# Kernel optimization log

Measured on AMD Instinct MI355X. Metric: run time of the kernel, lower is better.

Reference implementation:

```python
import jax, jax.numpy as jnp
import numpy as np

B, S, D = 8, 2048, 1024
NEG = -1000000000.0  # float32 masking constant from original code


def setup_inputs() -> dict:
    key = jax.random.key(0)
    kq, kk, kv, km = jax.random.split(key, 4)
    q = jax.random.normal(kq, (B, S, D), dtype=jnp.float32)
    k = jax.random.normal(kk, (B, S, D), dtype=jnp.float32)
    v = jax.random.normal(kv, (B, S, D), dtype=jnp.float32)
    mask = (jax.random.uniform(km, (B, 1, S)) < 0.1).astype(jnp.float32)
    return {"q": q, "k": k, "v": v, "mask": mask}


def reference(q, k, v, mask):
    scale = jnp.asarray(D ** -0.5, dtype=q.dtype)
    # [B,S,S] = q @ k^T, scaled
    logits = jnp.einsum("bqd,bkd->bqk", q, k) * scale
    logits = logits + mask * NEG  # mask broadcasts over query axis
    attn = jax.nn.softmax(logits, axis=-1)
    return jnp.einsum("bqk,bkd->bqd", attn, v)
```

## Files before the change

kernel.cpp:

```cpp
#include <hip/hip_runtime.h>
#include <hip/hip_bf16.h>

#define NB 8
#define SS 2048
#define DDIM 1024

typedef __attribute__((ext_vector_type(8))) short bf16x8;
typedef __attribute__((ext_vector_type(4))) float f32x4;

__device__ inline void gload_lds16(const void* g, void* l) {
  __builtin_amdgcn_global_load_lds(
      (const __attribute__((address_space(1))) void*)g,
      (__attribute__((address_space(3))) void*)l, 16, 0, 0);
}

__device__ inline ushort f2bf(float f) {
  union { float f; unsigned int u; } v;
  v.f = f;
  unsigned int u = v.u;
  unsigned int r = (u + 0x7FFFu + ((u >> 16) & 1u)) >> 16;
  return (ushort)r;
}

__device__ inline unsigned int pack2(float a, float b) {
  return (unsigned int)f2bf(a) | ((unsigned int)f2bf(b) << 16);
}

__global__ void init_zero(float* __restrict__ p, int n) {
  int i = blockIdx.x * 256 + threadIdx.x;
  if (i < n) p[i] = 0.f;
}

__global__ void conv_bf16(const float* __restrict__ in, ushort* __restrict__ out,
                          int n8) {
  int i = blockIdx.x * 256 + threadIdx.x;
  if (i >= n8) return;
  const float4* p = (const float4*)in + (size_t)i * 2;
  float4 a = p[0], b = p[1];
  uint4 o;
  o.x = pack2(a.x, a.y);
  o.y = pack2(a.z, a.w);
  o.z = pack2(b.x, b.y);
  o.w = pack2(b.z, b.w);
  ((uint4*)out)[i] = o;
}

__global__ void conv_transpose_v(const float* __restrict__ V,
                                 ushort* __restrict__ VT) {
  __shared__ ushort tile[64][65];
  const int b = blockIdx.z;
  const int k0 = blockIdx.x * 64;
  const int d0 = blockIdx.y * 64;
  const float* Vb = V + (size_t)b * SS * DDIM;
  ushort* VTb = VT + (size_t)b * DDIM * SS;
  const int t = threadIdx.x;
#pragma unroll
  for (int i = 0; i < 16; i++) {
    int flat = i * 256 + t;
    int r = flat >> 6, c = flat & 63;
    tile[r][c] = f2bf(Vb[(size_t)(k0 + r) * DDIM + d0 + c]);
  }
  __syncthreads();
#pragma unroll
  for (int i = 0; i < 16; i++) {
    int flat = i * 256 + t;
    int r = flat >> 6, c = flat & 63;
    VTb[(size_t)(d0 + r) * SS + k0 + c] = tile[c][r];
  }
}

template <bool EXPEPI, typename OutT>
__global__ void gemm_bt(const ushort* __restrict__ A, const ushort* __restrict__ Bm,
                        OutT* __restrict__ C, const float* __restrict__ maskp,
                        float* __restrict__ rowsum, int M, int N, int K,
                        float alpha) {
  __shared__ ushort lA[128 * 32];
  __shared__ ushort lB[128 * 32];
  const int tid = threadIdx.x;
  const int wave = tid >> 6, lane = tid & 63;
  const int quad = lane >> 4, l16 = lane & 15;
  const int wm = wave >> 1, wn = wave & 1;
  const int b = blockIdx.z;
  const ushort* Ab = A + (size_t)b * M * K;
  const ushort* Bb = Bm + (size_t)b * N * K;
  const int tileM = blockIdx.y * 128, tileN = blockIdx.x * 128;

  f32x4 acc[4][4];
#pragma unroll
  for (int i = 0; i < 4; i++)
#pragma unroll
    for (int j = 0; j < 4; j++) acc[i][j] = (f32x4){0.f, 0.f, 0.f, 0.f};

  for (int k0 = 0; k0 < K; k0 += 32) {
#pragma unroll
    for (int c = 0; c < 2; c++) {
      int flat = (wave * 2 + c) * 1024 + lane * 16;
      int row = flat >> 6, kb = flat & 63;
      gload_lds16((const char*)Ab + ((size_t)(tileM + row) * K + k0) * 2 + kb,
                  (char*)lA + flat);
      gload_lds16((const char*)Bb + ((size_t)(tileN + row) * K + k0) * 2 + kb,
                  (char*)lB + flat);
    }
    asm volatile("s_waitcnt vmcnt(0)" ::: "memory");
    __syncthreads();

    bf16x8 af[4], bfr[4];
#pragma unroll
    for (int mi = 0; mi < 4; mi++)
      af[mi] = *(const bf16x8*)((const char*)lA +
                                ((wm * 64 + mi * 16 + l16) * 32 + quad * 8) * 2);
#pragma unroll
    for (int ni = 0; ni < 4; ni++)
      bfr[ni] = *(const bf16x8*)((const char*)lB +
                                 ((wn * 64 + ni * 16 + l16) * 32 + quad * 8) * 2);
#pragma unroll
    for (int mi = 0; mi < 4; mi++)
#pragma unroll
      for (int ni = 0; ni < 4; ni++)
        acc[mi][ni] = __builtin_amdgcn_mfma_f32_16x16x32_bf16(af[mi], bfr[ni],
                                                              acc[mi][ni], 0, 0, 0);
    __syncthreads();
  }

  OutT* Cb = C + (size_t)b * M * N;
  if (EXPEPI) {
    const float* mb = maskp + (size_t)b * N;
    float mv[4];
#pragma unroll
    for (int ni = 0; ni < 4; ni++)
      mv[ni] = mb[tileN + wn * 64 + ni * 16 + l16] * (-1e9f);
#pragma unroll
    for (int mi = 0; mi < 4; mi++) {
#pragma unroll
      for (int r = 0; r < 4; r++) {
        int row = tileM + wm * 64 + mi * 16 + quad * 4 + r;
        float s = 0.f;
#pragma unroll
        for (int ni = 0; ni < 4; ni++) {
          int col = tileN + wn * 64 + ni * 16 + l16;
          float e = __expf(acc[mi][ni][r] * alpha + mv[ni]);
          ((ushort*)Cb)[(size_t)row * N + col] = f2bf(e);
          s += e;
        }
        s += __shfl_xor(s, 1, 64);
        s += __shfl_xor(s, 2, 64);
        s += __shfl_xor(s, 4, 64);
        s += __shfl_xor(s, 8, 64);
        if (l16 == 0) atomicAdd(&rowsum[(size_t)b * M + row], s);
      }
    }
  } else {
#pragma unroll
    for (int mi = 0; mi < 4; mi++) {
      float inv[4];
#pragma unroll
      for (int r = 0; r < 4; r++) {
        int row = tileM + wm * 64 + mi * 16 + quad * 4 + r;
        inv[r] = 1.0f / rowsum[(size_t)b * M + row];
      }
#pragma unroll
      for (int ni = 0; ni < 4; ni++) {
        int col = tileN + wn * 64 + ni * 16 + l16;
#pragma unroll
        for (int r = 0; r < 4; r++) {
          int row = tileM + wm * 64 + mi * 16 + quad * 4 + r;
          ((float*)Cb)[(size_t)row * N + col] = acc[mi][ni][r] * alpha * inv[r];
        }
      }
    }
  }
}

extern "C" void kernel_launch(void* const* d_in, const int* in_sizes, int n_in,
                              void* d_out, int out_size, void* d_ws, size_t ws_size,
                              hipStream_t stream) {
  const float* q = (const float*)d_in[0];
  const float* k = (const float*)d_in[1];
  const float* v = (const float*)d_in[2];
  const float* mask = (const float*)d_in[3];
  float* out = (float*)d_out;

  const size_t pQ = (size_t)SS * DDIM * 2;
  const size_t pP = (size_t)SS * SS * 2;
  const size_t pR = (size_t)SS * 4;

  int gb = 8;
  while (gb > 1 && (size_t)gb * (3 * pQ + pP + pR) > ws_size) gb >>= 1;

  for (int b0 = 0; b0 < NB; b0 += gb) {
    char* w = (char*)d_ws;
    ushort* qb = (ushort*)w;
    ushort* kb = (ushort*)(w + (size_t)gb * pQ);
    ushort* vtb = (ushort*)(w + (size_t)gb * pQ * 2);
    ushort* Sc = (ushort*)(w + (size_t)gb * pQ * 3);
    float* rowsum = (float*)(w + (size_t)gb * (pQ * 3 + pP));

    const float* qg = q + (size_t)b0 * SS * DDIM;
    const float* kg = k + (size_t)b0 * SS * DDIM;
    const float* vg = v + (size_t)b0 * SS * DDIM;
    const float* mg = mask + (size_t)b0 * SS;
    float* og = out + (size_t)b0 * SS * DDIM;

    const int nrs = gb * SS;
    init_zero<<<(nrs + 255) / 256, 256, 0, stream>>>(rowsum, nrs);
    const int n8 = gb * SS * DDIM / 8;
    conv_bf16<<<n8 / 256, 256, 0, stream>>>(qg, qb, n8);
    conv_bf16<<<n8 / 256, 256, 0, stream>>>(kg, kb, n8);
    conv_transpose_v<<<dim3(SS / 64, DDIM / 64, gb), 256, 0, stream>>>(vg, vtb);
    gemm_bt<true, ushort><<<dim3(SS / 128, SS / 128, gb), 256, 0, stream>>>(
        qb, kb, Sc, mg, rowsum, SS, SS, DDIM, 0.03125f);
    gemm_bt<false, float><<<dim3(DDIM / 128, SS / 128, gb), 256, 0, stream>>>(
        Sc, vtb, og, nullptr, rowsum, SS, DDIM, SS, 1.0f);
  }
}
```

Measured before the change: 412.0 us.

## Rewrite bf16 GEMMs with 256x256 tiles, double-buffered swizzled LDS and phased MFMA pipeline

Both GEMM kernels move from 128x128 tiles with 4 waves to 256x256 tiles with 8 waves. Global-to-LDS loads are double-buffered across 64-wide K steps, and each step is split into four barrier-separated quarter phases so loads for the next step overlap MFMA work. LDS rows are XOR-swizzled to avoid bank conflicts, and workgroup IDs are remapped across XCDs for cache locality. The aim is better data reuse and hiding of memory latency. The cost is 128KB of LDS per block, which limits occupancy to one block per CU, and fewer workgroups for the PV GEMM.

```diff
diff --git a/kernel.cpp b/kernel.cpp
--- a/kernel.cpp
+++ b/kernel.cpp
@@ -69,76 +69,158 @@
   }
 }
 
+#define MFMA16(mh, nh)                                                        \
+  _Pragma("unroll") for (int ks = 0; ks < 2; ks++)                            \
+  _Pragma("unroll") for (int mi = 0; mi < 4; mi++)                            \
+  _Pragma("unroll") for (int ni = 0; ni < 2; ni++)                            \
+      acc[mh][mi][nh][ni] = __builtin_amdgcn_mfma_f32_16x16x32_bf16(          \
+          af[mi][ks], bf[ni][ks], acc[mh][mi][nh][ni], 0, 0, 0);
+
+#define PHASE(mh, nh)                                                         \
+  __builtin_amdgcn_s_barrier();                                               \
+  asm volatile("s_waitcnt lgkmcnt(0)" ::: "memory");                          \
+  __builtin_amdgcn_sched_barrier(0);                                          \
+  __builtin_amdgcn_s_setprio(1);                                              \
+  MFMA16(mh, nh);                                                             \
+  __builtin_amdgcn_s_setprio(0);                                              \
+  __builtin_amdgcn_sched_barrier(0);
+
+#define VMW(n) asm volatile("s_waitcnt vmcnt(" #n ")" ::: "memory")
+#define ENDP() __builtin_amdgcn_s_barrier()
+
+#define RD_A(d, h)                                                            \
+  _Pragma("unroll") for (int mi = 0; mi < 4; mi++) {                          \
+    const char* _p = ldsc + (d) * 65536 + (h) * 16384 + aoff[mi];             \
+    af[mi][0] = *(const bf16x8*)(_p + koff0);                                 \
+    af[mi][1] = *(const bf16x8*)(_p + koff1);                                 \
+  }
+
+#define RD_B(d, h)                                                            \
+  _Pragma("unroll") for (int ni = 0; ni < 2; ni++) {                          \
+    const char* _p = ldsc + (d) * 65536 + 32768 + (h) * 16384 + boff[ni];     \
+    bf[ni][0] = *(const bf16x8*)(_p + koff0);                                 \
+    bf[ni][1] = *(const bf16x8*)(_p + koff1);                                 \
+  }
+
+#define STAGE(dbuf, isB, h, kt_)                                              \
+  do {                                                                        \
+    const ushort* _s = (isB) ? Bb : Ab;                                       \
+    const int _t0 = (isB) ? tileN : tileM;                                    \
+    char* _lb = ldsc + (dbuf) * 65536 + (isB) * 32768 + (h) * 16384;          \
+    gload_lds16(_s + (size_t)(_t0 + (h) * 128 + r0) * K + (kt_) * 64 + c8,    \
+                _lb + ol0);                                                   \
+    gload_lds16(_s + (size_t)(_t0 + (h) * 128 + r1) * K + (kt_) * 64 + c8,    \
+                _lb + ol1);                                                   \
+  } while (0)
+
 template <bool EXPEPI, typename OutT>
-__global__ void gemm_bt(const ushort* __restrict__ A, const ushort* __restrict__ Bm,
-                        OutT* __restrict__ C, const float* __restrict__ maskp,
-                        float* __restrict__ rowsum, int M, int N, int K,
-                        float alpha) {
-  __shared__ ushort lA[128 * 32];
-  __shared__ ushort lB[128 * 32];
+__global__ __launch_bounds__(512, 2) void gemm_bt(
+    const ushort* __restrict__ A, const ushort* __restrict__ Bm,
+    OutT* __restrict__ C, const float* __restrict__ maskp,
+    float* __restrict__ rowsum, int M, int N, int K, float alpha) {
+  __shared__ __attribute__((aligned(128))) char ldsc[131072];
   const int tid = threadIdx.x;
   const int wave = tid >> 6, lane = tid & 63;
   const int quad = lane >> 4, l16 = lane & 15;
-  const int wm = wave >> 1, wn = wave & 1;
-  const int b = blockIdx.z;
+  const int wm = wave >> 2, wn = wave & 3;
+
+  const int gx = gridDim.x, gy = gridDim.y;
+  const int lin = blockIdx.x + gx * (blockIdx.y + gy * blockIdx.z);
+  const int nwg = gx * gy * (int)gridDim.z;
+  const int cpx = nwg >> 3;
+  const int swz = (lin & 7) * cpx + (lin >> 3);
+  const int bz = swz / (gx * gy);
+  const int rem = swz - bz * (gx * gy);
+  const int by = rem / gx;
+  const int bx = rem - by * gx;
+
+  const int b = bz;
   const ushort* Ab = A + (size_t)b * M * K;
   const ushort* Bb = Bm + (size_t)b * N * K;
-  const int tileM = blockIdx.y * 128, tileN = blockIdx.x * 128;
-
-  f32x4 acc[4][4];
-#pragma unroll
-  for (int i = 0; i < 4; i++)
-#pragma unroll
-    for (int j = 0; j < 4; j++) acc[i][j] = (f32x4){0.f, 0.f, 0.f, 0.f};
-
-  for (int k0 = 0; k0 < K; k0 += 32) {
-#pragma unroll
-    for (int c = 0; c < 2; c++) {
-      int flat = (wave * 2 + c) * 1024 + lane * 16;
-      int row = flat >> 6, kb = flat & 63;
-      gload_lds16((const char*)Ab + ((size_t)(tileM + row) * K + k0) * 2 + kb,
-                  (char*)lA + flat);
-      gload_lds16((const char*)Bb + ((size_t)(tileN + row) * K + k0) * 2 + kb,
-                  (char*)lB + flat);
-    }
-    asm volatile("s_waitcnt vmcnt(0)" ::: "memory");
-    __syncthreads();
-
-    bf16x8 af[4], bfr[4];
+  const int tileM = by * 256, tileN = bx * 256;
+
+  const int ol0 = wave * 2048 + lane * 16;
+  const int ol1 = ol0 + 1024;
+  const int r0 = ol0 >> 7;
+  const int r1 = r0 + 8;
+  const int c8 = (((lane & 7) ^ (r0 & 7)) * 8);
+
+  const int x7 = lane & 7;
+  const int koff0 = ((quad) ^ x7) * 16;
+  const int koff1 = ((4 + quad) ^ x7) * 16;
+  int aoff[4], boff[2];
+#pragma unroll
+  for (int mi = 0; mi < 4; mi++) aoff[mi] = (wm * 64 + mi * 16 + l16) * 128;
+#pragma unroll
+  for (int ni = 0; ni < 2; ni++) boff[ni] = (wn * 32 + ni * 16 + l16) * 128;
+
+  f32x4 acc[2][4][2][2];
+#pragma unroll
+  for (int mh = 0; mh < 2; mh++)
 #pragma unroll
     for (int mi = 0; mi < 4; mi++)
-      af[mi] = *(const bf16x8*)((const char*)lA +
-                                ((wm * 64 + mi * 16 + l16) * 32 + quad * 8) * 2);
-#pragma unroll
-    for (int ni = 0; ni < 4; ni++)
-      bfr[ni] = *(const bf16x8*)((const char*)lB +
-                                 ((wn * 64 + ni * 16 + l16) * 32 + quad * 8) * 2);
-#pragma unroll
-    for (int mi = 0; mi < 4; mi++)
-#pragma unroll
-      for (int ni = 0; ni < 4; ni++)
-        acc[mi][ni] = __builtin_amdgcn_mfma_f32_16x16x32_bf16(af[mi], bfr[ni],
-                                                              acc[mi][ni], 0, 0, 0);
-    __syncthreads();
+#pragma unroll
+      for (int nh = 0; nh < 2; nh++)
+#pragma unroll
+        for (int ni = 0; ni < 2; ni++)
+          acc[mh][mi][nh][ni] = (f32x4){0.f, 0.f, 0.f, 0.f};
+
+  bf16x8 af[4][2], bf[2][2];
+  const int NKT = K >> 6;
+
+  STAGE(0, 0, 0, 0);
+  STAGE(0, 1, 0, 0);
+  STAGE(0, 1, 1, 0);
+  STAGE(0, 0, 1, 0);
+  VMW(4);
+  __builtin_amdgcn_s_barrier();
+
+  for (int kt = 0; kt < NKT - 1; ++kt) {
+    const int d = kt & 1, dn = d ^ 1;
+    RD_A(d, 0); RD_B(d, 0); STAGE(dn, 0, 0, kt + 1);
+    PHASE(0, 0); VMW(4); ENDP();
+    RD_B(d, 1);             STAGE(dn, 1, 0, kt + 1);
+    PHASE(0, 1); VMW(4); ENDP();
+    RD_A(d, 1);             STAGE(dn, 1, 1, kt + 1);
+    PHASE(1, 1); ENDP();
+    RD_B(d, 0);             STAGE(dn, 0, 1, kt + 1);
+    PHASE(1, 0); VMW(4); ENDP();
+  }
+  {
+    const int d = (NKT - 1) & 1;
+    RD_A(d, 0); RD_B(d, 0);
+    PHASE(0, 0); VMW(2); ENDP();
+    RD_B(d, 1);
+    PHASE(0, 1); VMW(0); ENDP();
+    RD_A(d, 1);
+    PHASE(1, 1); ENDP();
+    RD_B(d, 0);
+    PHASE(1, 0); ENDP();
   }
 
   OutT* Cb = C + (size_t)b * M * N;
   if (EXPEPI) {
     const float* mb = maskp + (size_t)b * N;
-    float mv[4];
-#pragma unroll
-    for (int ni = 0; ni < 4; ni++)
-      mv[ni] = mb[tileN + wn * 64 + ni * 16 + l16] * (-1e9f);
+    float mv[2][2];
+#pragma unroll
+    for (int nh = 0; nh < 2; nh++)
+#pragma unroll
+      for (int ni = 0; ni < 2; ni++)
+        mv[nh][ni] = mb[tileN + nh * 128 + wn * 32 + ni * 16 + l16] * (-1e9f);
+#pragma unroll
+    for (int mh = 0; mh < 2; mh++)
 #pragma unroll
     for (int mi = 0; mi < 4; mi++) {
 #pragma unroll
-      for (int r = 0; r < 4; r++) {
-        int row = tileM + wm * 64 + mi * 16 + quad * 4 + r;
+      for (int rr = 0; rr < 4; rr++) {
+        const int row = tileM + mh * 128 + wm * 64 + mi * 16 + quad * 4 + rr;
         float s = 0.f;
 #pragma unroll
-        for (int ni = 0; ni < 4; ni++) {
-          int col = tileN + wn * 64 + ni * 16 + l16;
-          float e = __expf(acc[mi][ni][r] * alpha + mv[ni]);
+        for (int nh = 0; nh < 2; nh++)
+#pragma unroll
+        for (int ni = 0; ni < 2; ni++) {
+          const int col = tileN + nh * 128 + wn * 32 + ni * 16 + l16;
+          float e = __expf(acc[mh][mi][nh][ni][rr] * alpha + mv[nh][ni]);
           ((ushort*)Cb)[(size_t)row * N + col] = f2bf(e);
           s += e;
         }
@@ -151,20 +233,25 @@
     }
   } else {
 #pragma unroll
+    for (int mh = 0; mh < 2; mh++)
+#pragma unroll
     for (int mi = 0; mi < 4; mi++) {
       float inv[4];
 #pragma unroll
-      for (int r = 0; r < 4; r++) {
-        int row = tileM + wm * 64 + mi * 16 + quad * 4 + r;
-        inv[r] = 1.0f / rowsum[(size_t)b * M + row];
+      for (int rr = 0; rr < 4; rr++) {
+        const int row = tileM + mh * 128 + wm * 64 + mi * 16 + quad * 4 + rr;
+        inv[rr] = 1.0f / rowsum[(size_t)b * M + row];
       }
 #pragma unroll
-      for (int ni = 0; ni < 4; ni++) {
-        int col = tileN + wn * 64 + ni * 16 + l16;
-#pragma unroll
-        for (int r = 0; r < 4; r++) {
-          int row = tileM + wm * 64 + mi * 16 + quad * 4 + r;
-          ((float*)Cb)[(size_t)row * N + col] = acc[mi][ni][r] * alpha * inv[r];
+      for (int nh = 0; nh < 2; nh++)
+#pragma unroll
+      for (int ni = 0; ni < 2; ni++) {
+        const int col = tileN + nh * 128 + wn * 32 + ni * 16 + l16;
+#pragma unroll
+        for (int rr = 0; rr < 4; rr++) {
+          const int row = tileM + mh * 128 + wm * 64 + mi * 16 + quad * 4 + rr;
+          ((float*)Cb)[(size_t)row * N + col] =
+              acc[mh][mi][nh][ni][rr] * alpha * inv[rr];
         }
       }
     }
@@ -207,9 +294,9 @@
     conv_bf16<<<n8 / 256, 256, 0, stream>>>(qg, qb, n8);
     conv_bf16<<<n8 / 256, 256, 0, stream>>>(kg, kb, n8);
     conv_transpose_v<<<dim3(SS / 64, DDIM / 64, gb), 256, 0, stream>>>(vg, vtb);
-    gemm_bt<true, ushort><<<dim3(SS / 128, SS / 128, gb), 256, 0, stream>>>(
+    gemm_bt<true, ushort><<<dim3(SS / 256, SS / 256, gb), 512, 0, stream>>>(
         qb, kb, Sc, mg, rowsum, SS, SS, DDIM, 0.03125f);
-    gemm_bt<false, float><<<dim3(DDIM / 128, SS / 128, gb), 256, 0, stream>>>(
+    gemm_bt<false, float><<<dim3(DDIM / 256, SS / 256, gb), 512, 0, stream>>>(
         Sc, vtb, og, nullptr, rowsum, SS, DDIM, SS, 1.0f);
   }
 }
```

Result: faster. 368.4 us (-10.6%).
